# Optimization experiments

Measured on AMD Instinct MI355X. Metric: run time of the kernel, lower is better.

Reference implementation:

```python
import jax, jax.numpy as jnp
import numpy as np

B, C, H, W = 8, 64, 128, 128
OUT, K, PAD = 128, 9, 1  # 3x3 kernel -> K=9 taps


def setup_inputs() -> dict:
    key = jax.random.key(0)
    ks = jax.random.split(key, 6)
    x = jax.random.normal(ks[0], (B, C, H, W), dtype=jnp.float32)
    # trained-like params: small random offsets (std ~1-2 px) and mask logits
    w_offset = jax.random.normal(ks[1], (2 * K, C, 3, 3), dtype=jnp.float32) * 0.05
    b_offset = jax.random.normal(ks[2], (2 * K,), dtype=jnp.float32) * 0.1
    w_mask = jax.random.normal(ks[3], (K, C, 3, 3), dtype=jnp.float32) * 0.05
    b_mask = jax.random.normal(ks[4], (K,), dtype=jnp.float32) * 0.1
    w_conv = jax.random.normal(ks[5], (OUT, C, 3, 3), dtype=jnp.float32) * (1.0 / np.sqrt(C * 9))
    return {"x": x, "w_offset": w_offset, "b_offset": b_offset,
            "w_mask": w_mask, "b_mask": b_mask, "w_conv": w_conv}


def _conv3x3(x, w, b):
    out = jax.lax.conv_general_dilated(
        x, w, window_strides=(1, 1), padding=((PAD, PAD), (PAD, PAD)),
        dimension_numbers=("NCHW", "OIHW", "NCHW"))
    return out + b[None, :, None, None]


def _bilinear_gather(img, gy, gx):
    # img: [C,H,W]; gy,gx: [K,H,W] float sampling coords (zero outside bounds)
    C_, H_, W_ = img.shape
    y0 = jnp.floor(gy)
    x0 = jnp.floor(gx)
    wy = gy - y0
    wx = gx - x0
    img_flat = img.reshape(C_, H_ * W_)

    def corner(yi, xi, wgt):
        valid = ((yi >= 0) & (yi < H_) & (xi >= 0) & (xi < W_)).astype(img.dtype)
        yc = jnp.clip(yi, 0, H_ - 1).astype(jnp.int32)
        xc = jnp.clip(xi, 0, W_ - 1).astype(jnp.int32)
        v = img_flat[:, yc * W_ + xc]  # [C,K,H,W]
        return v * (wgt * valid)[None]

    return (corner(y0, x0, (1 - wy) * (1 - wx))
            + corner(y0, x0 + 1, (1 - wy) * wx)
            + corner(y0 + 1, x0, wy * (1 - wx))
            + corner(y0 + 1, x0 + 1, wy * wx))  # [C,K,H,W]


def reference(x, w_offset, b_offset, w_mask, b_mask, w_conv):
    offset = _conv3x3(x, w_offset, b_offset)                  # [B,18,H,W]
    mask = jax.nn.sigmoid(_conv3x3(x, w_mask, b_mask))        # [B,9,H,W]
    B_, C_, H_, W_ = x.shape
    # torchvision layout: channel 2k = dy, 2k+1 = dx for kernel tap k
    off = offset.reshape(B_, K, 2, H_, W_)
    dy, dx = off[:, :, 0], off[:, :, 1]                       # [B,K,H,W]
    ky, kx = jnp.meshgrid(jnp.arange(3, dtype=x.dtype),
                          jnp.arange(3, dtype=x.dtype), indexing="ij")
    gy = jnp.arange(H_, dtype=x.dtype)[None, None, :, None] - PAD + ky.reshape(1, K, 1, 1) + dy
    gx = jnp.arange(W_, dtype=x.dtype)[None, None, None, :] - PAD + kx.reshape(1, K, 1, 1) + dx
    sampled = jax.vmap(_bilinear_gather)(x, gy, gx)           # [B,C,K,H,W]
    sampled = sampled * mask[:, None]                         # modulated (DCNv2)
    out = jnp.einsum("bckhw,ock->bohw", sampled, w_conv.reshape(OUT, C_, K))
    return out
```

## Files before the change

kernel.cpp:

```cpp
#include <hip/hip_runtime.h>
#include <math.h>

#define Himg 128
#define Wimg 128
#define HW   16384
#define Cin  64
#define Kk   9
#define OUTC 128
#define Bsz  8

typedef __attribute__((ext_vector_type(8))) _Float16 half8;
typedef __attribute__((ext_vector_type(4))) float   floatx4;

__global__ __launch_bounds__(256) void transpose_x(const float* __restrict__ x,
                                                   _Float16* __restrict__ xt) {
    __shared__ _Float16 tile[Cin][130];
    int t   = threadIdx.x;
    int bid = blockIdx.x;
    int b   = bid >> 7;
    int h   = bid & 127;
    const float* xb = x + (size_t)b * Cin * HW + (size_t)h * Wimg;
#pragma unroll
    for (int j = 0; j < 32; ++j) {
        int e = t + j * 256;
        int c = e >> 7;
        int w = e & 127;
        tile[c][w] = (_Float16)xb[(size_t)c * HW + w];
    }
    __syncthreads();
    unsigned* dst = (unsigned*)xt + ((size_t)b * HW + (size_t)h * Wimg) * 32;
#pragma unroll
    for (int j = 0; j < 16; ++j) {
        int d  = t + j * 256;
        int w  = d >> 5;
        int cp = d & 31;
        union { unsigned u; _Float16 hh[2]; } pk;
        pk.hh[0] = tile[2 * cp][w];
        pk.hh[1] = tile[2 * cp + 1][w];
        dst[d] = pk.u;
    }
}

__global__ __launch_bounds__(256) void repack_w(const float* __restrict__ w_conv,
                                                _Float16* __restrict__ wpk_h) {
    int idx = blockIdx.x * 256 + threadIdx.x;
    if (idx >= Kk * Cin * OUTC) return;
    int i    = idx & 7;
    int l    = (idx >> 3) & 63;
    int g    = idx >> 9;
    int mt   = g & 7;
    int ch   = g >> 3;
    int kq   = l >> 4;
    int ln16 = l & 15;
    int o    = mt * 16 + ln16;
    int kl   = kq * 8 + i;
    int c    = (ch & 1) * 32 + kl;
    int kt   = ch >> 1;
    wpk_h[idx] = (_Float16)w_conv[(o * Cin + c) * 9 + kt];
}

__global__ __launch_bounds__(256) void repack_w2(const float* __restrict__ w_offset,
                                                 const float* __restrict__ w_mask,
                                                 _Float16* __restrict__ wpk2) {
    int idx = blockIdx.x * 256 + threadIdx.x;
    if (idx >= 18 * 32 * 32) return;
    int i    = idx & 7;
    int l    = (idx >> 3) & 63;
    int g    = idx >> 9;
    int mt0  = g & 1;
    int ch   = g >> 1;
    int kq   = l >> 4;
    int ln16 = l & 15;
    int m    = mt0 * 16 + ln16;
    int kl   = kq * 8 + i;
    int c    = (ch & 1) * 32 + kl;
    int kt   = ch >> 1;
    float v = 0.0f;
    if (m < 18)      v = w_offset[(m * Cin + c) * 9 + kt];
    else if (m < 27) v = w_mask[((m - 18) * Cin + c) * 9 + kt];
    wpk2[idx] = (_Float16)v;
}

__global__ __launch_bounds__(256, 3) void deform_fused(
        const _Float16* __restrict__ xt, const _Float16* __restrict__ wpk_h,
        const _Float16* __restrict__ wpk2,
        const float* __restrict__ b_offset, const float* __restrict__ b_mask,
        float* __restrict__ out) {
    __shared__ union SMem {
        struct { _Float16 V0[2][64][40]; float P[32][66]; } p0;
        struct { _Float16 V[2][64][40]; } p1;
    } sm;

    int t    = threadIdx.x;
    int bid  = blockIdx.x;
    int b    = bid & 7;
    int pb   = bid >> 3;
    int pix0 = pb * 64;
    int h    = pix0 >> 7;
    int w0   = pix0 & 127;

    int lane = t & 63;
    int wv   = t >> 6;
    int q    = t >> 2;
    int c4   = t & 3;
    int kq   = lane >> 4;
    int ln16 = lane & 15;

    const _Float16* xtb  = xt + (size_t)b * HW * Cin;
    const half8* wsrc    = (const half8*)wpk_h;
    const half8* w2src   = (const half8*)wpk2;

    floatx4 acc2[2];
    acc2[0] = (floatx4){0.f, 0.f, 0.f, 0.f};
    acc2[1] = (floatx4){0.f, 0.f, 0.f, 0.f};
    int mt0 = wv & 1;
    int ntA = wv >> 1;

    half8 pv, af;
    {
        int row = h - 1, col = w0 + q - 1;
        bool okc = (row >= 0) && (col >= 0) && (col < Wimg);
        if (okc) pv = *(const half8*)(xtb + ((size_t)(row * Wimg + col)) * Cin + c4 * 8);
        else {
#pragma unroll
            for (int i = 0; i < 8; ++i) pv[i] = (_Float16)0.f;
        }
        af = w2src[(size_t)mt0 * 64 + lane];
    }

#pragma unroll
    for (int ch = 0; ch < 18; ++ch) {
        int buf = ch & 1;
        *(half8*)&sm.p0.V0[buf][q][c4 * 8] = pv;
        half8 afc = af;
        if (ch < 17) {
            int chn = ch + 1, ktn = chn >> 1, cgn = chn & 1;
            int row = h + (ktn / 3) - 1;
            int col = w0 + q + (ktn % 3) - 1;
            bool okc = (row >= 0) && (row < Himg) && (col >= 0) && (col < Wimg);
            if (okc) pv = *(const half8*)(xtb + ((size_t)(row * Wimg + col)) * Cin
                                          + cgn * 32 + c4 * 8);
            else {
#pragma unroll
                for (int i = 0; i < 8; ++i) pv[i] = (_Float16)0.f;
            }
            af = w2src[((size_t)chn * 2 + mt0) * 64 + lane];
        }
        __syncthreads();
        half8 b0 = *(const half8*)&sm.p0.V0[buf][ntA * 16 + ln16][kq * 8];
        half8 b1 = *(const half8*)&sm.p0.V0[buf][(ntA + 2) * 16 + ln16][kq * 8];
        acc2[0] = __builtin_amdgcn_mfma_f32_16x16x32_f16(afc, b0, acc2[0], 0, 0, 0);
        acc2[1] = __builtin_amdgcn_mfma_f32_16x16x32_f16(afc, b1, acc2[1], 0, 0, 0);
    }
#pragma unroll
    for (int j = 0; j < 2; ++j) {
        int nt = ntA + 2 * j;
#pragma unroll
        for (int r = 0; r < 4; ++r)
            sm.p0.P[mt0 * 16 + kq * 4 + r][nt * 16 + ln16] = acc2[j][r];
    }
    __syncthreads();

    int      o00r[9], packr[9];
    unsigned wab[9], wcd[9];
    {
        float fh = (float)h, fw = (float)(w0 + q);
#pragma unroll
        for (int k = 0; k < 9; ++k) {
            float dyv = sm.p0.P[2 * k][q]     + b_offset[2 * k];
            float dxv = sm.p0.P[2 * k + 1][q] + b_offset[2 * k + 1];
            float mz  = sm.p0.P[18 + k][q]    + b_mask[k];
            float mkv = 1.0f / (1.0f + expf(-mz));

            float gy  = fh + (float)(k / 3) - 1.0f + dyv;
            float gx  = fw + (float)(k % 3) - 1.0f + dxv;
            float y0f = floorf(gy), x0f = floorf(gx);
            int   y0  = (int)y0f,   x0 = (int)x0f;
            float wy  = gy - y0f,   wx = gx - x0f;
            int   y1  = y0 + 1,     x1 = x0 + 1;

            bool vy0 = (y0 >= 0) && (y0 < Himg);
            bool vy1 = (y1 >= 0) && (y1 < Himg);
            bool vx0 = (x0 >= 0) && (x0 < Wimg);
            bool vx1 = (x1 >= 0) && (x1 < Wimg);

            float w00 = (vy0 && vx0) ? (1.0f - wy) * (1.0f - wx) * mkv : 0.0f;
            float w01 = (vy0 && vx1) ? (1.0f - wy) * wx          * mkv : 0.0f;
            float w10 = (vy1 && vx0) ? wy          * (1.0f - wx) * mkv : 0.0f;
            float w11 = (vy1 && vx1) ? wy          * wx          * mkv : 0.0f;

            int y0c = min(max(y0, 0), Himg - 1), y1c = min(max(y1, 0), Himg - 1);
            int x0c = min(max(x0, 0), Wimg - 1), x1c = min(max(x1, 0), Wimg - 1);
            o00r[k]  = y0c * Wimg + x0c;
            packr[k] = (x1c - x0c) | ((y1c - y0c) << 16);
            union { unsigned u; _Float16 hh[2]; } pk;
            pk.hh[0] = (_Float16)w00; pk.hh[1] = (_Float16)w01; wab[k] = pk.u;
            pk.hh[0] = (_Float16)w10; pk.hh[1] = (_Float16)w11; wcd[k] = pk.u;
        }
    }

    floatx4 acc[2][4];
#pragma unroll
    for (int i = 0; i < 2; ++i)
#pragma unroll
        for (int j = 0; j < 4; ++j) acc[i][j] = (floatx4){0.f, 0.f, 0.f, 0.f};
    int m0 = wv * 32;

    half8 ga, gb, gc, gd, ar0, ar1;
    {
        int o00 = o00r[0], pk = packr[0];
        const _Float16* xc = xtb + (size_t)o00 * Cin + c4 * 8;
        int ob = (pk & 0xffff) << 6;
        int oc = (pk >> 16) << 13;
        ga = *(const half8*)(xc);
        gb = *(const half8*)(xc + ob);
        gc = *(const half8*)(xc + oc);
        gd = *(const half8*)(xc + oc + ob);
        ar0 = wsrc[(size_t)(2 * wv) * 64 + lane];
        ar1 = wsrc[(size_t)(2 * wv + 1) * 64 + lane];
    }
    __syncthreads();

#pragma unroll
    for (int ch = 0; ch < 18; ++ch) {
        int kt  = ch >> 1;
        int buf = ch & 1;
        union { unsigned u; _Float16 hh[2]; } u1, u2;
        u1.u = wab[kt];  u2.u = wcd[kt];
        float w00 = (float)u1.hh[0], w01 = (float)u1.hh[1];
        float w10 = (float)u2.hh[0], w11 = (float)u2.hh[1];
        half8 vv;
#pragma unroll
        for (int i = 0; i < 8; ++i) {
            float v = w00 * (float)ga[i] + w01 * (float)gb[i] +
                      w10 * (float)gc[i] + w11 * (float)gd[i];
            vv[i] = (_Float16)v;
        }
        *(half8*)&sm.p1.V[buf][q][c4 * 8] = vv;
        half8 a0c = ar0, a1c = ar1;
        if (ch < 17) {
            int chn = ch + 1, ktn = chn >> 1, cgn = chn & 1;
            int o00 = o00r[ktn], pk = packr[ktn];
            const _Float16* xc = xtb + (size_t)o00 * Cin + cgn * 32 + c4 * 8;
            int ob = (pk & 0xffff) << 6;
            int oc = (pk >> 16) << 13;
            ga = *(const half8*)(xc);
            gb = *(const half8*)(xc + ob);
            gc = *(const half8*)(xc + oc);
            gd = *(const half8*)(xc + oc + ob);
            ar0 = wsrc[((size_t)chn * 8 + 2 * wv) * 64 + lane];
            ar1 = wsrc[((size_t)chn * 8 + 2 * wv + 1) * 64 + lane];
        }
        __syncthreads();
#pragma unroll
        for (int nt = 0; nt < 4; ++nt) {
            half8 bf = *(const half8*)&sm.p1.V[buf][nt * 16 + ln16][kq * 8];
            acc[0][nt] = __builtin_amdgcn_mfma_f32_16x16x32_f16(a0c, bf, acc[0][nt], 0, 0, 0);
            acc[1][nt] = __builtin_amdgcn_mfma_f32_16x16x32_f16(a1c, bf, acc[1][nt], 0, 0, 0);
        }
    }

#pragma unroll
    for (int mtl = 0; mtl < 2; ++mtl) {
#pragma unroll
        for (int nt = 0; nt < 4; ++nt) {
#pragma unroll
            for (int r = 0; r < 4; ++r) {
                int o  = m0 + mtl * 16 + kq * 4 + r;
                int px = nt * 16 + ln16;
                out[(size_t)(b * OUTC + o) * HW + pix0 + px] = acc[mtl][nt][r];
            }
        }
    }
}

extern "C" void kernel_launch(void* const* d_in, const int* in_sizes, int n_in,
                              void* d_out, int out_size, void* d_ws, size_t ws_size,
                              hipStream_t stream) {
    const float* x        = (const float*)d_in[0];
    const float* w_offset = (const float*)d_in[1];
    const float* b_offset = (const float*)d_in[2];
    const float* w_mask   = (const float*)d_in[3];
    const float* b_mask   = (const float*)d_in[4];
    const float* w_conv   = (const float*)d_in[5];
    float* out = (float*)d_out;

    _Float16* wpk_h = (_Float16*)d_ws;
    _Float16* wpk2  = wpk_h + 73728;
    _Float16* xtb   = wpk2 + 18432;

    transpose_x<<<1024, 256, 0, stream>>>(x, xtb);
    repack_w<<<288, 256, 0, stream>>>(w_conv, wpk_h);
    repack_w2<<<72, 256, 0, stream>>>(w_offset, w_mask, wpk2);
    deform_fused<<<2048, 256, 0, stream>>>(xtb, wpk_h, wpk2, b_offset, b_mask, out);
}
```

Measured before the change: 176.4 us.

## Merge prep kernels, deepen gather prefetch, use packed fp16 bilinear, raise occupancy

```diff
diff --git a/kernel.cpp b/kernel.cpp
--- a/kernel.cpp
+++ b/kernel.cpp
@@ -12,76 +12,87 @@
 typedef __attribute__((ext_vector_type(8))) _Float16 half8;
 typedef __attribute__((ext_vector_type(4))) float   floatx4;
 
-__global__ __launch_bounds__(256) void transpose_x(const float* __restrict__ x,
-                                                   _Float16* __restrict__ xt) {
+#define SPL8(v) ((half8){(v),(v),(v),(v),(v),(v),(v),(v)})
+
+__global__ __launch_bounds__(256) void prep(const float* __restrict__ x,
+                                            const float* __restrict__ w_conv,
+                                            const float* __restrict__ w_offset,
+                                            const float* __restrict__ w_mask,
+                                            _Float16* __restrict__ xt,
+                                            _Float16* __restrict__ wpk_h,
+                                            _Float16* __restrict__ wpk2) {
     __shared__ _Float16 tile[Cin][130];
     int t   = threadIdx.x;
     int bid = blockIdx.x;
-    int b   = bid >> 7;
-    int h   = bid & 127;
-    const float* xb = x + (size_t)b * Cin * HW + (size_t)h * Wimg;
-#pragma unroll
-    for (int j = 0; j < 32; ++j) {
-        int e = t + j * 256;
-        int c = e >> 7;
-        int w = e & 127;
-        tile[c][w] = (_Float16)xb[(size_t)c * HW + w];
-    }
-    __syncthreads();
-    unsigned* dst = (unsigned*)xt + ((size_t)b * HW + (size_t)h * Wimg) * 32;
-#pragma unroll
-    for (int j = 0; j < 16; ++j) {
-        int d  = t + j * 256;
-        int w  = d >> 5;
-        int cp = d & 31;
-        union { unsigned u; _Float16 hh[2]; } pk;
-        pk.hh[0] = tile[2 * cp][w];
-        pk.hh[1] = tile[2 * cp + 1][w];
-        dst[d] = pk.u;
+
+    if (bid < 1024) {
+        int b = bid >> 7;
+        int h = bid & 127;
+        const float* xb = x + (size_t)b * Cin * HW + (size_t)h * Wimg;
+#pragma unroll
+        for (int j = 0; j < 32; ++j) {
+            int e = t + j * 256;
+            int c = e >> 7;
+            int w = e & 127;
+            tile[c][w] = (_Float16)xb[(size_t)c * HW + w];
+        }
+        __syncthreads();
+        unsigned* dst = (unsigned*)xt + ((size_t)b * HW + (size_t)h * Wimg) * 32;
+#pragma unroll
+        for (int j = 0; j < 16; ++j) {
+            int d  = t + j * 256;
+            int w  = d >> 5;
+            int cp = d & 31;
+            union { unsigned u; _Float16 hh[2]; } pk;
+            pk.hh[0] = tile[2 * cp][w];
+            pk.hh[1] = tile[2 * cp + 1][w];
+            dst[d] = pk.u;
+        }
+        return;
+    }
+
+    if (bid < 1024 + 288) {
+        int idx = (bid - 1024) * 256 + t;
+        if (idx < Kk * Cin * OUTC) {
+            int i    = idx & 7;
+            int l    = (idx >> 3) & 63;
+            int g    = idx >> 9;
+            int mt   = g & 7;
+            int ch   = g >> 3;
+            int kq   = l >> 4;
+            int ln16 = l & 15;
+            int o    = mt * 16 + ln16;
+            int kl   = kq * 8 + i;
+            int c    = (ch & 1) * 32 + kl;
+            int kt   = ch >> 1;
+            wpk_h[idx] = (_Float16)w_conv[(o * Cin + c) * 9 + kt];
+        }
+        return;
+    }
+
+    {
+        int idx = (bid - 1312) * 256 + t;
+        if (idx < 18 * 32 * 32) {
+            int i    = idx & 7;
+            int l    = (idx >> 3) & 63;
+            int g    = idx >> 9;
+            int mt0  = g & 1;
+            int ch   = g >> 1;
+            int kq   = l >> 4;
+            int ln16 = l & 15;
+            int m    = mt0 * 16 + ln16;
+            int kl   = kq * 8 + i;
+            int c    = (ch & 1) * 32 + kl;
+            int kt   = ch >> 1;
+            float v = 0.0f;
+            if (m < 18)      v = w_offset[(m * Cin + c) * 9 + kt];
+            else if (m < 27) v = w_mask[((m - 18) * Cin + c) * 9 + kt];
+            wpk2[idx] = (_Float16)v;
+        }
     }
 }
 
-__global__ __launch_bounds__(256) void repack_w(const float* __restrict__ w_conv,
-                                                _Float16* __restrict__ wpk_h) {
-    int idx = blockIdx.x * 256 + threadIdx.x;
-    if (idx >= Kk * Cin * OUTC) return;
-    int i    = idx & 7;
-    int l    = (idx >> 3) & 63;
-    int g    = idx >> 9;
-    int mt   = g & 7;
-    int ch   = g >> 3;
-    int kq   = l >> 4;
-    int ln16 = l & 15;
-    int o    = mt * 16 + ln16;
-    int kl   = kq * 8 + i;
-    int c    = (ch & 1) * 32 + kl;
-    int kt   = ch >> 1;
-    wpk_h[idx] = (_Float16)w_conv[(o * Cin + c) * 9 + kt];
-}
-
-__global__ __launch_bounds__(256) void repack_w2(const float* __restrict__ w_offset,
-                                                 const float* __restrict__ w_mask,
-                                                 _Float16* __restrict__ wpk2) {
-    int idx = blockIdx.x * 256 + threadIdx.x;
-    if (idx >= 18 * 32 * 32) return;
-    int i    = idx & 7;
-    int l    = (idx >> 3) & 63;
-    int g    = idx >> 9;
-    int mt0  = g & 1;
-    int ch   = g >> 1;
-    int kq   = l >> 4;
-    int ln16 = l & 15;
-    int m    = mt0 * 16 + ln16;
-    int kl   = kq * 8 + i;
-    int c    = (ch & 1) * 32 + kl;
-    int kt   = ch >> 1;
-    float v = 0.0f;
-    if (m < 18)      v = w_offset[(m * Cin + c) * 9 + kt];
-    else if (m < 27) v = w_mask[((m - 18) * Cin + c) * 9 + kt];
-    wpk2[idx] = (_Float16)v;
-}
-
-__global__ __launch_bounds__(256, 3) void deform_fused(
+__global__ __launch_bounds__(256, 4) void deform_fused(
         const _Float16* __restrict__ xt, const _Float16* __restrict__ wpk_h,
         const _Float16* __restrict__ wpk2,
         const float* __restrict__ b_offset, const float* __restrict__ b_mask,
@@ -116,36 +127,30 @@
     int mt0 = wv & 1;
     int ntA = wv >> 1;
 
-    half8 pv, af;
-    {
-        int row = h - 1, col = w0 + q - 1;
-        bool okc = (row >= 0) && (col >= 0) && (col < Wimg);
-        if (okc) pv = *(const half8*)(xtb + ((size_t)(row * Wimg + col)) * Cin + c4 * 8);
+    half8 pv[2], af;
+    auto loadx0 = [&](int chn, half8& dst) {
+        int ktn = chn >> 1, cgn = chn & 1;
+        int row = h + (ktn / 3) - 1;
+        int col = w0 + q + (ktn % 3) - 1;
+        bool okc = (row >= 0) && (row < Himg) && (col >= 0) && (col < Wimg);
+        if (okc) dst = *(const half8*)(xtb + ((size_t)(row * Wimg + col)) * Cin
+                                       + cgn * 32 + c4 * 8);
         else {
 #pragma unroll
-            for (int i = 0; i < 8; ++i) pv[i] = (_Float16)0.f;
-        }
-        af = w2src[(size_t)mt0 * 64 + lane];
-    }
+            for (int i = 0; i < 8; ++i) dst[i] = (_Float16)0.f;
+        }
+    };
+    loadx0(0, pv[0]);
+    loadx0(1, pv[1]);
+    af = w2src[(size_t)mt0 * 64 + lane];
 
 #pragma unroll
     for (int ch = 0; ch < 18; ++ch) {
         int buf = ch & 1;
-        *(half8*)&sm.p0.V0[buf][q][c4 * 8] = pv;
+        *(half8*)&sm.p0.V0[buf][q][c4 * 8] = pv[buf];
         half8 afc = af;
-        if (ch < 17) {
-            int chn = ch + 1, ktn = chn >> 1, cgn = chn & 1;
-            int row = h + (ktn / 3) - 1;
-            int col = w0 + q + (ktn % 3) - 1;
-            bool okc = (row >= 0) && (row < Himg) && (col >= 0) && (col < Wimg);
-            if (okc) pv = *(const half8*)(xtb + ((size_t)(row * Wimg + col)) * Cin
-                                          + cgn * 32 + c4 * 8);
-            else {
-#pragma unroll
-                for (int i = 0; i < 8; ++i) pv[i] = (_Float16)0.f;
-            }
-            af = w2src[((size_t)chn * 2 + mt0) * 64 + lane];
-        }
+        if (ch < 16) loadx0(ch + 2, pv[buf]);
+        if (ch < 17) af = w2src[((size_t)(ch + 1) * 2 + mt0) * 64 + lane];
         __syncthreads();
         half8 b0 = *(const half8*)&sm.p0.V0[buf][ntA * 16 + ln16][kq * 8];
         half8 b1 = *(const half8*)&sm.p0.V0[buf][(ntA + 2) * 16 + ln16][kq * 8];
@@ -206,19 +211,22 @@
         for (int j = 0; j < 4; ++j) acc[i][j] = (floatx4){0.f, 0.f, 0.f, 0.f};
     int m0 = wv * 32;
 
-    half8 ga, gb, gc, gd, ar0, ar1;
-    {
-        int o00 = o00r[0], pk = packr[0];
-        const _Float16* xc = xtb + (size_t)o00 * Cin + c4 * 8;
+    half8 g[2][4], ar0, ar1;
+    auto loadg = [&](int chn, half8* dst) {
+        int ktn = chn >> 1, cgn = chn & 1;
+        int o00 = o00r[ktn], pk = packr[ktn];
+        const _Float16* xc = xtb + (size_t)o00 * Cin + cgn * 32 + c4 * 8;
         int ob = (pk & 0xffff) << 6;
         int oc = (pk >> 16) << 13;
-        ga = *(const half8*)(xc);
-        gb = *(const half8*)(xc + ob);
-        gc = *(const half8*)(xc + oc);
-        gd = *(const half8*)(xc + oc + ob);
-        ar0 = wsrc[(size_t)(2 * wv) * 64 + lane];
-        ar1 = wsrc[(size_t)(2 * wv + 1) * 64 + lane];
-    }
+        dst[0] = *(const half8*)(xc);
+        dst[1] = *(const half8*)(xc + ob);
+        dst[2] = *(const half8*)(xc + oc);
+        dst[3] = *(const half8*)(xc + oc + ob);
+    };
+    loadg(0, g[0]);
+    loadg(1, g[1]);
+    ar0 = wsrc[(size_t)(2 * wv) * 64 + lane];
+    ar1 = wsrc[(size_t)(2 * wv + 1) * 64 + lane];
     __syncthreads();
 
 #pragma unroll
@@ -227,29 +235,14 @@
         int buf = ch & 1;
         union { unsigned u; _Float16 hh[2]; } u1, u2;
         u1.u = wab[kt];  u2.u = wcd[kt];
-        float w00 = (float)u1.hh[0], w01 = (float)u1.hh[1];
-        float w10 = (float)u2.hh[0], w11 = (float)u2.hh[1];
-        half8 vv;
-#pragma unroll
-        for (int i = 0; i < 8; ++i) {
-            float v = w00 * (float)ga[i] + w01 * (float)gb[i] +
-                      w10 * (float)gc[i] + w11 * (float)gd[i];
-            vv[i] = (_Float16)v;
-        }
+        half8 vv = g[buf][0] * SPL8(u1.hh[0]) + g[buf][1] * SPL8(u1.hh[1])
+                 + g[buf][2] * SPL8(u2.hh[0]) + g[buf][3] * SPL8(u2.hh[1]);
         *(half8*)&sm.p1.V[buf][q][c4 * 8] = vv;
         half8 a0c = ar0, a1c = ar1;
+        if (ch < 16) loadg(ch + 2, g[buf]);
         if (ch < 17) {
-            int chn = ch + 1, ktn = chn >> 1, cgn = chn & 1;
-            int o00 = o00r[ktn], pk = packr[ktn];
-            const _Float16* xc = xtb + (size_t)o00 * Cin + cgn * 32 + c4 * 8;
-            int ob = (pk & 0xffff) << 6;
-            int oc = (pk >> 16) << 13;
-            ga = *(const half8*)(xc);
-            gb = *(const half8*)(xc + ob);
-            gc = *(const half8*)(xc + oc);
-            gd = *(const half8*)(xc + oc + ob);
-            ar0 = wsrc[((size_t)chn * 8 + 2 * wv) * 64 + lane];
-            ar1 = wsrc[((size_t)chn * 8 + 2 * wv + 1) * 64 + lane];
+            ar0 = wsrc[((size_t)(ch + 1) * 8 + 2 * wv) * 64 + lane];
+            ar1 = wsrc[((size_t)(ch + 1) * 8 + 2 * wv + 1) * 64 + lane];
         }
         __syncthreads();
 #pragma unroll
@@ -289,8 +282,6 @@
     _Float16* wpk2  = wpk_h + 73728;
     _Float16* xtb   = wpk2 + 18432;
 
-    transpose_x<<<1024, 256, 0, stream>>>(x, xtb);
-    repack_w<<<288, 256, 0, stream>>>(w_conv, wpk_h);
-    repack_w2<<<72, 256, 0, stream>>>(w_offset, w_mask, wpk2);
+    prep<<<1384, 256, 0, stream>>>(x, w_conv, w_offset, w_mask, xtb, wpk_h, wpk2);
     deform_fused<<<2048, 256, 0, stream>>>(xtb, wpk_h, wpk2, b_offset, b_mask, out);
 }
```

New measurement: 177.4 us. Within noise of the previous version (+0.6%).
